# Performance work log

Hardware: AMD Instinct MI355X
Metric: run time of the kernel (lower is better)

The kernel has to match this reference:

```python
import jax, jax.numpy as jnp
import numpy as np
from jax import lax

K = 33  # avgpool kernel
P = 16  # padding
EPS = 1e-08


def _box_sum(x):
    # Sum over 33x33 windows, stride 1, zero padding 16 on H and W (NCHW).
    return lax.reduce_window(
        x, 0.0, lax.add,
        window_dimensions=(1, 1, K, K),
        window_strides=(1, 1, 1, 1),
        padding=((0, 0), (0, 0), (P, P), (P, P)),
    )


def setup_inputs() -> dict:
    key = jax.random.key(0)
    input_tensor = jax.random.normal(key, (64, 1, 80, 3000), dtype=jnp.float32)
    return {"input_tensor": input_tensor}


def reference(input_tensor):
    B, C, H, W = input_tensor.shape
    # count_include_pad=False: divide by number of VALID elements per window.
    counts = _box_sum(jnp.ones((1, 1, H, W), dtype=input_tensor.dtype))
    local_mean = _box_sum(input_tensor) / counts
    centered = input_tensor - local_mean
    local_var = _box_sum(centered * centered) / counts
    local_std = jnp.sqrt(local_var)
    return centered / (local_std + EPS)
```

## Files before the change

### kernel.cpp

```cpp
#include <hip/hip_runtime.h>
#include <hip/hip_bf16.h>
#include <math.h>

#define BB 64
#define HH 80
#define WW 3000
#define RAD 16
#define TW 80
#define NLOAD 112
#define XSW 112
#define HXS 116
#define NSTRIP 38
#define NT 1024
#define EPSF 1e-8f

#define XS_WORDS (HH * XSW)
#define HXP_OFF  XS_WORDS
#define HXP_WORDS (TW * HXS)
#define ICH_OFF  (XS_WORDS + HXP_WORDS)
#define TOT_WORDS (ICH_OFF + HH)

typedef float f32x2 __attribute__((ext_vector_type(2)));
typedef float f32x4 __attribute__((ext_vector_type(4)));

__device__ __forceinline__ float bflo(uint32_t w) { return __uint_as_float(w << 16); }
__device__ __forceinline__ float bfhi(uint32_t w) { return __uint_as_float(w & 0xffff0000u); }
__device__ __forceinline__ uint32_t packbf2(float lo, float hi) {
    union { __hip_bfloat162 h2; uint32_t u; } u;
    u.h2 = __hip_bfloat162(__float2bfloat16(lo), __float2bfloat16(hi));
    return u.u;
}
__device__ __forceinline__ f32x2 uw(uint32_t w) {
    f32x2 r; r.x = bflo(w); r.y = bfhi(w); return r;
}

#if defined(__has_builtin)
#if __has_builtin(__builtin_amdgcn_global_load_lds)
#define HAVE_GLL 1
__device__ __forceinline__ void gload_lds16(const float* g, float* l) {
    __builtin_amdgcn_global_load_lds(
        (const __attribute__((address_space(1))) void*)g,
        (__attribute__((address_space(3))) void*)l, 16, 0, 0);
}
#endif
#endif

#define E4(V, J) ((J) == 0 ? (V).x : ((J) == 1 ? (V).y : ((J) == 2 ? (V).z : (V).w)))
#define F48(Q) E4((Q) < 4 ? G0 : (Q) < 8 ? G1 : (Q) < 12 ? G2 : (Q) < 16 ? G3 : (Q) < 20 ? G4 : \
                  (Q) < 24 ? G5 : (Q) < 28 ? G6 : (Q) < 32 ? G7 : (Q) < 36 ? G8 : \
                  (Q) < 40 ? G9 : (Q) < 44 ? G10 : G11, (Q) & 3)
#define W48(Q) E4((Q) < 4 ? R0 : (Q) < 8 ? R1 : (Q) < 12 ? R2 : (Q) < 16 ? R3 : (Q) < 20 ? R4 : \
                  (Q) < 24 ? R5 : (Q) < 28 ? R6 : (Q) < 32 ? R7 : (Q) < 36 ? R8 : \
                  (Q) < 40 ? R9 : (Q) < 44 ? R10 : R11, (Q) & 3)
#define F16(K) E4((K) < 4 ? f0 : (K) < 8 ? f1 : (K) < 12 ? f2 : f3, (K) & 3)

__global__ __launch_bounds__(NT, 8)
void localnorm_kernel(const float* __restrict__ in, float* __restrict__ out) {
    extern __shared__ uint32_t smem[];
    float*    smemf = (float*)smem;
    uint32_t* Hxp   = smem + HXP_OFF;
    float*   inv_ch = (float*)(smem + ICH_OFF);

    const int t     = threadIdx.x;
    const int strip = blockIdx.x % NSTRIP;
    const int b     = blockIdx.x / NSTRIP;
    const int c0    = strip * TW;
    const float* inb = in + (size_t)b * (HH * WW);

    if (t < HH) {
        int lo = max(t - RAD, 0), hi = min(t + RAD, HH - 1);
        inv_ch[t] = 1.0f / (float)(hi - lo + 1);
    }
    if (t < 640) {
        const int col = t >> 3;
        const int c8  = t & 7;
        const int off = col * HXS + ((c8 < 4) ? (c8 * 4) : (96 + (c8 - 4) * 4));
        *(uint4*)(Hxp + off) = make_uint4(0u, 0u, 0u, 0u);
    }

    bool dma = false;
#ifdef HAVE_GLL
    dma = (c0 >= 16) && (c0 + NLOAD - 16 <= WW);
#endif
    if (dma) {
#ifdef HAVE_GLL
        const float* gsrc = inb + (c0 - 16);
        #pragma unroll
        for (int i = 0; i < 3; ++i) {
            const int ck = t + i * NT;
            if (i < 2 || ck < 2240) {
                const int row = ck / 28;
                const int m   = ck - row * 28;
                gload_lds16(gsrc + (size_t)row * WW + 4 * m, smemf + 4 * ck);
            }
        }
#endif
    } else {
        #pragma unroll
        for (int it = 0; it < 3; ++it) {
            const int id = t + it * NT;
            if (it < 2 || id < 2240) {
                const int row = id / 28;
                const int q   = id - row * 28;
                const int gc  = c0 - 16 + 4 * q;
                const float* rp = inb + (size_t)row * WW;
                f32x4 v;
                if (gc >= 0 && gc + 4 <= WW) {
                    v = *(const f32x4*)(rp + gc);
                } else {
                    v.x = (gc     >= 0 && gc     < WW) ? rp[gc]     : 0.f;
                    v.y = (gc + 1 >= 0 && gc + 1 < WW) ? rp[gc + 1] : 0.f;
                    v.z = (gc + 2 >= 0 && gc + 2 < WW) ? rp[gc + 2] : 0.f;
                    v.w = (gc + 3 >= 0 && gc + 3 < WW) ? rp[gc + 3] : 0.f;
                }
                *(f32x4*)(smemf + row * XSW + 4 * q) = v;
            }
        }
    }
    __syncthreads();

    {
        const int row = t % HH;
        const int seg = t / HH;
        if (seg < 5) {
            const float* xr = smemf + row * XSW + seg * 16;
            f32x4 G0  = *(const f32x4*)(xr);
            f32x4 G1  = *(const f32x4*)(xr + 4);
            f32x4 G2  = *(const f32x4*)(xr + 8);
            f32x4 G3  = *(const f32x4*)(xr + 12);
            f32x4 G4  = *(const f32x4*)(xr + 16);
            f32x4 G5  = *(const f32x4*)(xr + 20);
            f32x4 G6  = *(const f32x4*)(xr + 24);
            f32x4 G7  = *(const f32x4*)(xr + 28);
            f32x4 G8  = *(const f32x4*)(xr + 32);
            f32x4 G9  = *(const f32x4*)(xr + 36);
            f32x4 G10 = *(const f32x4*)(xr + 40);
            f32x4 G11 = *(const f32x4*)(xr + 44);
            float e32 = F48(32);
            float axA = e32, axB = 0.f;
            float qxA = e32 * e32, qxB = 0.f;
            #pragma unroll
            for (int q = 0; q < 32; q += 2) {
                float fa = F48(q), fb = F48(q + 1);
                axA += fa;                 axB += fb;
                qxA = fmaf(fa, fa, qxA);   qxB = fmaf(fb, fb, qxB);
            }
            float ax = axA + axB, axx = qxA + qxB;
            uint32_t* hw = Hxp + (seg * 16) * HXS + row + 16;
            #pragma unroll
            for (int k = 0; k < 8; ++k) {
                float fs = F48(2 * k), fe = F48(2 * k + 33);
                float a1x  = ax - fs + fe;
                float a1xx = fmaf(fe, fe, fmaf(-fs, fs, axx));
                hw[(2 * k) * HXS]     = packbf2(ax, axx);
                hw[(2 * k + 1) * HXS] = packbf2(a1x, a1xx);
                if (k != 7) {
                    float fs2 = F48(2 * k + 1), fe2 = F48(2 * k + 34);
                    ax  = a1x - fs2 + fe2;
                    axx = fmaf(fe2, fe2, fmaf(-fs2, fs2, a1xx));
                }
            }
        }
    }
    __syncthreads();

    {
        const int c    = t % TW;
        const int band = t / TW;
        const int gc   = c0 + c;
        if (band < 5 && gc < WW) {
            const int r0 = band * 16;
            const uint32_t* hp = Hxp + c * HXS + r0;
            uint4 R0  = *(const uint4*)(hp);
            uint4 R1  = *(const uint4*)(hp + 4);
            uint4 R2  = *(const uint4*)(hp + 8);
            uint4 R3  = *(const uint4*)(hp + 12);
            uint4 R4  = *(const uint4*)(hp + 16);
            uint4 R5  = *(const uint4*)(hp + 20);
            uint4 R6  = *(const uint4*)(hp + 24);
            uint4 R7  = *(const uint4*)(hp + 28);
            uint4 R8  = *(const uint4*)(hp + 32);
            uint4 R9  = *(const uint4*)(hp + 36);
            uint4 R10 = *(const uint4*)(hp + 40);
            uint4 R11 = *(const uint4*)(hp + 44);
            f32x2 aA = uw(W48(32));
            f32x2 aB; aB.x = 0.f; aB.y = 0.f;
            #pragma unroll
            for (int q = 0; q < 32; q += 2) {
                aA += uw(W48(q));
                aB += uw(W48(q + 1));
            }
            f32x2 acc = aA + aB;
            const float icw = 1.0f / (float)(min(gc + RAD, WW - 1) - max(gc - RAD, 0) + 1);
            f32x4 f0 = *(const f32x4*)(inv_ch + r0);
            f32x4 f1 = *(const f32x4*)(inv_ch + r0 + 4);
            f32x4 f2 = *(const f32x4*)(inv_ch + r0 + 8);
            f32x4 f3 = *(const f32x4*)(inv_ch + r0 + 12);
            float* outb = out + (size_t)b * (HH * WW);
            #pragma unroll
            for (int k = 0; k < 16; ++k) {
                const int r = r0 + k;
                const float ninv = F16(k) * icw;
                f32x2 me = acc * ninv;
                float var = fmaxf(me.y - me.x * me.x, 1e-24f);
#if defined(__has_builtin) && __has_builtin(__builtin_amdgcn_rsqf)
                float isd = __builtin_amdgcn_rsqf(var);
#else
                float isd = __builtin_amdgcn_rcpf(__builtin_amdgcn_sqrtf(var) + EPSF);
#endif
                float xv = smemf[r * XSW + c + 16];
                outb[(size_t)r * WW + gc] = (xv - me.x) * isd;
                if (k != 15) {
                    acc += uw(W48(k + 33)) - uw(W48(k));
                }
            }
        }
    }
}

extern "C" void kernel_launch(void* const* d_in, const int* in_sizes, int n_in,
                              void* d_out, int out_size, void* d_ws, size_t ws_size,
                              hipStream_t stream) {
    const float* in = (const float*)d_in[0];
    float* out = (float*)d_out;

    const size_t lds_bytes = (size_t)TOT_WORDS * sizeof(uint32_t);
    static bool attr_set = false;
    if (!attr_set) {
        (void)hipFuncSetAttribute((const void*)localnorm_kernel,
                                  hipFuncAttributeMaxDynamicSharedMemorySize,
                                  (int)lds_bytes);
        attr_set = true;
    }

    dim3 grid(BB * NSTRIP);
    dim3 block(NT);
    localnorm_kernel<<<grid, block, lds_bytes, stream>>>(in, out);
}
```

Baseline: 35.76 us.

## Use persistent blocks with double-buffered async prefetch of narrower strips

Converts the one-block-per-strip launch into a persistent grid of 512 blocks that loop over work items. Each block prefetches the next strip's input into a second LDS buffer with global_load_lds while it computes the current strip. Strip width drops from 80 to 48 columns, so the 32-column halo is a larger fraction of each load. Only 3 of 16 waves run the horizontal pass and 10 run the vertical pass, so thread utilisation per phase falls and redundant halo reads grow, in exchange for overlapping load latency with compute.

Measured after the change: 45.52 us. +27.3%, slower.

```diff
diff --git a/kernel.cpp b/kernel.cpp
--- a/kernel.cpp
+++ b/kernel.cpp
@@ -6,18 +6,20 @@
 #define HH 80
 #define WW 3000
 #define RAD 16
-#define TW 80
-#define NLOAD 112
-#define XSW 112
+#define TW 48
+#define NLOAD 80
+#define XSW 80
 #define HXS 116
-#define NSTRIP 38
+#define NSTRIP 63
+#define NITEMS (BB * NSTRIP)
+#define NBLK 512
 #define NT 1024
 #define EPSF 1e-8f
 
-#define XS_WORDS (HH * XSW)
-#define HXP_OFF  XS_WORDS
-#define HXP_WORDS (TW * HXS)
-#define ICH_OFF  (XS_WORDS + HXP_WORDS)
+#define XSA_OFF 0
+#define XSB_OFF (HH * XSW)
+#define HXP_OFF (2 * HH * XSW)
+#define ICH_OFF (HXP_OFF + TW * HXS)
 #define TOT_WORDS (ICH_OFF + HH)
 
 typedef float f32x2 __attribute__((ext_vector_type(2)));
@@ -45,14 +47,54 @@
 #endif
 #endif
 
+__device__ __forceinline__ void stage_item(const float* __restrict__ in, int w, float* xbuf, int t) {
+    const int b     = w / NSTRIP;
+    const int strip = w - b * NSTRIP;
+    const int c0    = strip * TW;
+    const float* inb = in + (size_t)b * (HH * WW);
+#ifdef HAVE_GLL
+    if ((c0 >= 16) && (c0 - 16 + NLOAD <= WW)) {
+        const float* gsrc = inb + (c0 - 16);
+        {
+            const int ck = t;
+            const int row = ck / 20, m = ck - row * 20;
+            gload_lds16(gsrc + (size_t)row * WW + 4 * m, xbuf + 4 * ck);
+        }
+        if (t < 576) {
+            const int ck = t + NT;
+            const int row = ck / 20, m = ck - row * 20;
+            gload_lds16(gsrc + (size_t)row * WW + 4 * m, xbuf + 4 * ck);
+        }
+        return;
+    }
+#endif
+    #pragma unroll
+    for (int it = 0; it < 2; ++it) {
+        const int id = t + it * NT;
+        if (it == 0 || id < 1600) {
+            const int row = id / 20, q = id - row * 20;
+            const int gc  = c0 - 16 + 4 * q;
+            const float* rp = inb + (size_t)row * WW;
+            f32x4 v;
+            if (gc >= 0 && gc + 4 <= WW) {
+                v = *(const f32x4*)(rp + gc);
+            } else {
+                v.x = (gc     >= 0 && gc     < WW) ? rp[gc]     : 0.f;
+                v.y = (gc + 1 >= 0 && gc + 1 < WW) ? rp[gc + 1] : 0.f;
+                v.z = (gc + 2 >= 0 && gc + 2 < WW) ? rp[gc + 2] : 0.f;
+                v.w = (gc + 3 >= 0 && gc + 3 < WW) ? rp[gc + 3] : 0.f;
+            }
+            *(f32x4*)(xbuf + 4 * id) = v;
+        }
+    }
+}
+
 #define E4(V, J) ((J) == 0 ? (V).x : ((J) == 1 ? (V).y : ((J) == 2 ? (V).z : (V).w)))
 #define F48(Q) E4((Q) < 4 ? G0 : (Q) < 8 ? G1 : (Q) < 12 ? G2 : (Q) < 16 ? G3 : (Q) < 20 ? G4 : \
                   (Q) < 24 ? G5 : (Q) < 28 ? G6 : (Q) < 32 ? G7 : (Q) < 36 ? G8 : \
                   (Q) < 40 ? G9 : (Q) < 44 ? G10 : G11, (Q) & 3)
-#define W48(Q) E4((Q) < 4 ? R0 : (Q) < 8 ? R1 : (Q) < 12 ? R2 : (Q) < 16 ? R3 : (Q) < 20 ? R4 : \
-                  (Q) < 24 ? R5 : (Q) < 28 ? R6 : (Q) < 32 ? R7 : (Q) < 36 ? R8 : \
-                  (Q) < 40 ? R9 : (Q) < 44 ? R10 : R11, (Q) & 3)
-#define F16(K) E4((K) < 4 ? f0 : (K) < 8 ? f1 : (K) < 12 ? f2 : f3, (K) & 3)
+#define W40(Q) E4((Q) < 4 ? v0 : (Q) < 8 ? v1 : (Q) < 12 ? v2 : (Q) < 16 ? v3 : (Q) < 20 ? v4 : \
+                  (Q) < 24 ? v5 : (Q) < 28 ? v6 : (Q) < 32 ? v7 : (Q) < 36 ? v8 : v9, (Q) & 3)
 
 __global__ __launch_bounds__(NT, 8)
 void localnorm_kernel(const float* __restrict__ in, float* __restrict__ out) {
@@ -60,161 +102,132 @@
     float*    smemf = (float*)smem;
     uint32_t* Hxp   = smem + HXP_OFF;
     float*   inv_ch = (float*)(smem + ICH_OFF);
-
-    const int t     = threadIdx.x;
-    const int strip = blockIdx.x % NSTRIP;
-    const int b     = blockIdx.x / NSTRIP;
-    const int c0    = strip * TW;
-    const float* inb = in + (size_t)b * (HH * WW);
+    float*   XsA    = smemf + XSA_OFF;
+    float*   XsB    = smemf + XSB_OFF;
+
+    const int t   = threadIdx.x;
+    const int bid = blockIdx.x;
 
     if (t < HH) {
         int lo = max(t - RAD, 0), hi = min(t + RAD, HH - 1);
         inv_ch[t] = 1.0f / (float)(hi - lo + 1);
     }
-    if (t < 640) {
+    if (t < 384) {
         const int col = t >> 3;
         const int c8  = t & 7;
         const int off = col * HXS + ((c8 < 4) ? (c8 * 4) : (96 + (c8 - 4) * 4));
         *(uint4*)(Hxp + off) = make_uint4(0u, 0u, 0u, 0u);
     }
 
-    bool dma = false;
-#ifdef HAVE_GLL
-    dma = (c0 >= 16) && (c0 + NLOAD - 16 <= WW);
-#endif
-    if (dma) {
-#ifdef HAVE_GLL
-        const float* gsrc = inb + (c0 - 16);
-        #pragma unroll
-        for (int i = 0; i < 3; ++i) {
-            const int ck = t + i * NT;
-            if (i < 2 || ck < 2240) {
-                const int row = ck / 28;
-                const int m   = ck - row * 28;
-                gload_lds16(gsrc + (size_t)row * WW + 4 * m, smemf + 4 * ck);
+    stage_item(in, bid, XsA, t);
+    __syncthreads();
+
+    int cur = 0;
+    #pragma unroll 1
+    for (int w = bid; w < NITEMS; w += NBLK) {
+        float* Xs = cur ? XsB : XsA;
+        float* Xn = cur ? XsA : XsB;
+        if (w + NBLK < NITEMS) stage_item(in, w + NBLK, Xn, t);
+
+        const int b     = w / NSTRIP;
+        const int strip = w - b * NSTRIP;
+        const int c0    = strip * TW;
+
+        {
+            const int row = t % HH;
+            const int seg = t / HH;
+            if (seg < 3) {
+                const float* xr = Xs + row * XSW + seg * 16;
+                f32x4 G0  = *(const f32x4*)(xr);
+                f32x4 G1  = *(const f32x4*)(xr + 4);
+                f32x4 G2  = *(const f32x4*)(xr + 8);
+                f32x4 G3  = *(const f32x4*)(xr + 12);
+                f32x4 G4  = *(const f32x4*)(xr + 16);
+                f32x4 G5  = *(const f32x4*)(xr + 20);
+                f32x4 G6  = *(const f32x4*)(xr + 24);
+                f32x4 G7  = *(const f32x4*)(xr + 28);
+                f32x4 G8  = *(const f32x4*)(xr + 32);
+                f32x4 G9  = *(const f32x4*)(xr + 36);
+                f32x4 G10 = *(const f32x4*)(xr + 40);
+                f32x4 G11 = *(const f32x4*)(xr + 44);
+                float e32 = F48(32);
+                float axA = e32, axB = 0.f;
+                float qxA = e32 * e32, qxB = 0.f;
+                #pragma unroll
+                for (int q = 0; q < 32; q += 2) {
+                    float fa = F48(q), fb = F48(q + 1);
+                    axA += fa;                 axB += fb;
+                    qxA = fmaf(fa, fa, qxA);   qxB = fmaf(fb, fb, qxB);
+                }
+                float ax = axA + axB, axx = qxA + qxB;
+                uint32_t* hw = Hxp + (seg * 16) * HXS + row + 16;
+                #pragma unroll
+                for (int k = 0; k < 8; ++k) {
+                    float fs = F48(2 * k), fe = F48(2 * k + 33);
+                    float a1x  = ax - fs + fe;
+                    float a1xx = fmaf(fe, fe, fmaf(-fs, fs, axx));
+                    hw[(2 * k) * HXS]     = packbf2(ax, axx);
+                    hw[(2 * k + 1) * HXS] = packbf2(a1x, a1xx);
+                    if (k != 7) {
+                        float fs2 = F48(2 * k + 1), fe2 = F48(2 * k + 34);
+                        ax  = a1x - fs2 + fe2;
+                        axx = fmaf(fe2, fe2, fmaf(-fs2, fs2, a1xx));
+                    }
+                }
             }
         }
-#endif
-    } else {
-        #pragma unroll
-        for (int it = 0; it < 3; ++it) {
-            const int id = t + it * NT;
-            if (it < 2 || id < 2240) {
-                const int row = id / 28;
-                const int q   = id - row * 28;
-                const int gc  = c0 - 16 + 4 * q;
-                const float* rp = inb + (size_t)row * WW;
-                f32x4 v;
-                if (gc >= 0 && gc + 4 <= WW) {
-                    v = *(const f32x4*)(rp + gc);
-                } else {
-                    v.x = (gc     >= 0 && gc     < WW) ? rp[gc]     : 0.f;
-                    v.y = (gc + 1 >= 0 && gc + 1 < WW) ? rp[gc + 1] : 0.f;
-                    v.z = (gc + 2 >= 0 && gc + 2 < WW) ? rp[gc + 2] : 0.f;
-                    v.w = (gc + 3 >= 0 && gc + 3 < WW) ? rp[gc + 3] : 0.f;
-                }
-                *(f32x4*)(smemf + row * XSW + 4 * q) = v;
+        __syncthreads();
+
+        {
+            const int c    = t % TW;
+            const int band = t / TW;
+            const int gc   = c0 + c;
+            if (band < 10 && gc < WW) {
+                const int r0 = band * 8;
+                const uint32_t* hp = Hxp + c * HXS + r0;
+                uint4 v0 = *(const uint4*)(hp);
+                uint4 v1 = *(const uint4*)(hp + 4);
+                uint4 v2 = *(const uint4*)(hp + 8);
+                uint4 v3 = *(const uint4*)(hp + 12);
+                uint4 v4 = *(const uint4*)(hp + 16);
+                uint4 v5 = *(const uint4*)(hp + 20);
+                uint4 v6 = *(const uint4*)(hp + 24);
+                uint4 v7 = *(const uint4*)(hp + 28);
+                uint4 v8 = *(const uint4*)(hp + 32);
+                uint4 v9 = *(const uint4*)(hp + 36);
+                f32x2 aA = uw(W40(32));
+                f32x2 aB; aB.x = 0.f; aB.y = 0.f;
+                #pragma unroll
+                for (int q = 0; q < 32; q += 2) {
+                    aA += uw(W40(q));
+                    aB += uw(W40(q + 1));
+                }
+                f32x2 acc = aA + aB;
+                const float icw = 1.0f / (float)(min(gc + RAD, WW - 1) - max(gc - RAD, 0) + 1);
+                f32x4 f4a = *(const f32x4*)(inv_ch + r0);
+                f32x4 f4b = *(const f32x4*)(inv_ch + r0 + 4);
+                float* outb = out + (size_t)b * (HH * WW);
+                #pragma unroll
+                for (int k = 0; k < 8; ++k) {
+                    const int r = r0 + k;
+                    const float ninv = E4(k < 4 ? f4a : f4b, k & 3) * icw;
+                    f32x2 me = acc * ninv;
+                    float var = fmaxf(me.y - me.x * me.x, 1e-24f);
+#if defined(__has_builtin) && __has_builtin(__builtin_amdgcn_rsqf)
+                    float isd = __builtin_amdgcn_rsqf(var);
+#else
+                    float isd = __builtin_amdgcn_rcpf(__builtin_amdgcn_sqrtf(var) + EPSF);
+#endif
+                    float xv = Xs[r * XSW + c + 16];
+                    outb[(size_t)r * WW + gc] = (xv - me.x) * isd;
+                    if (k != 7) {
+                        acc += uw(W40(k + 33)) - uw(W40(k));
+                    }
+                }
             }
         }
-    }
-    __syncthreads();
-
-    {
-        const int row = t % HH;
-        const int seg = t / HH;
-        if (seg < 5) {
-            const float* xr = smemf + row * XSW + seg * 16;
-            f32x4 G0  = *(const f32x4*)(xr);
-            f32x4 G1  = *(const f32x4*)(xr + 4);
-            f32x4 G2  = *(const f32x4*)(xr + 8);
-            f32x4 G3  = *(const f32x4*)(xr + 12);
-            f32x4 G4  = *(const f32x4*)(xr + 16);
-            f32x4 G5  = *(const f32x4*)(xr + 20);
-            f32x4 G6  = *(const f32x4*)(xr + 24);
-            f32x4 G7  = *(const f32x4*)(xr + 28);
-            f32x4 G8  = *(const f32x4*)(xr + 32);
-            f32x4 G9  = *(const f32x4*)(xr + 36);
-            f32x4 G10 = *(const f32x4*)(xr + 40);
-            f32x4 G11 = *(const f32x4*)(xr + 44);
-            float e32 = F48(32);
-            float axA = e32, axB = 0.f;
-            float qxA = e32 * e32, qxB = 0.f;
-            #pragma unroll
-            for (int q = 0; q < 32; q += 2) {
-                float fa = F48(q), fb = F48(q + 1);
-                axA += fa;                 axB += fb;
-                qxA = fmaf(fa, fa, qxA);   qxB = fmaf(fb, fb, qxB);
-            }
-            float ax = axA + axB, axx = qxA + qxB;
-            uint32_t* hw = Hxp + (seg * 16) * HXS + row + 16;
-            #pragma unroll
-            for (int k = 0; k < 8; ++k) {
-                float fs = F48(2 * k), fe = F48(2 * k + 33);
-                float a1x  = ax - fs + fe;
-                float a1xx = fmaf(fe, fe, fmaf(-fs, fs, axx));
-                hw[(2 * k) * HXS]     = packbf2(ax, axx);
-                hw[(2 * k + 1) * HXS] = packbf2(a1x, a1xx);
-                if (k != 7) {
-                    float fs2 = F48(2 * k + 1), fe2 = F48(2 * k + 34);
-                    ax  = a1x - fs2 + fe2;
-                    axx = fmaf(fe2, fe2, fmaf(-fs2, fs2, a1xx));
-                }
-            }
-        }
-    }
-    __syncthreads();
-
-    {
-        const int c    = t % TW;
-        const int band = t / TW;
-        const int gc   = c0 + c;
-        if (band < 5 && gc < WW) {
-            const int r0 = band * 16;
-            const uint32_t* hp = Hxp + c * HXS + r0;
-            uint4 R0  = *(const uint4*)(hp);
-            uint4 R1  = *(const uint4*)(hp + 4);
-            uint4 R2  = *(const uint4*)(hp + 8);
-            uint4 R3  = *(const uint4*)(hp + 12);
-            uint4 R4  = *(const uint4*)(hp + 16);
-            uint4 R5  = *(const uint4*)(hp + 20);
-            uint4 R6  = *(const uint4*)(hp + 24);
-            uint4 R7  = *(const uint4*)(hp + 28);
-            uint4 R8  = *(const uint4*)(hp + 32);
-            uint4 R9  = *(const uint4*)(hp + 36);
-            uint4 R10 = *(const uint4*)(hp + 40);
-            uint4 R11 = *(const uint4*)(hp + 44);
-            f32x2 aA = uw(W48(32));
-            f32x2 aB; aB.x = 0.f; aB.y = 0.f;
-            #pragma unroll
-            for (int q = 0; q < 32; q += 2) {
-                aA += uw(W48(q));
-                aB += uw(W48(q + 1));
-            }
-            f32x2 acc = aA + aB;
-            const float icw = 1.0f / (float)(min(gc + RAD, WW - 1) - max(gc - RAD, 0) + 1);
-            f32x4 f0 = *(const f32x4*)(inv_ch + r0);
-            f32x4 f1 = *(const f32x4*)(inv_ch + r0 + 4);
-            f32x4 f2 = *(const f32x4*)(inv_ch + r0 + 8);
-            f32x4 f3 = *(const f32x4*)(inv_ch + r0 + 12);
-            float* outb = out + (size_t)b * (HH * WW);
-            #pragma unroll
-            for (int k = 0; k < 16; ++k) {
-                const int r = r0 + k;
-                const float ninv = F16(k) * icw;
-                f32x2 me = acc * ninv;
-                float var = fmaxf(me.y - me.x * me.x, 1e-24f);
-#if defined(__has_builtin) && __has_builtin(__builtin_amdgcn_rsqf)
-                float isd = __builtin_amdgcn_rsqf(var);
-#else
-                float isd = __builtin_amdgcn_rcpf(__builtin_amdgcn_sqrtf(var) + EPSF);
-#endif
-                float xv = smemf[r * XSW + c + 16];
-                outb[(size_t)r * WW + gc] = (xv - me.x) * isd;
-                if (k != 15) {
-                    acc += uw(W48(k + 33)) - uw(W48(k));
-                }
-            }
-        }
+        __syncthreads();
+        cur ^= 1;
     }
 }
 
@@ -233,7 +246,7 @@
         attr_set = true;
     }
 
-    dim3 grid(BB * NSTRIP);
+    dim3 grid(NBLK);
     dim3 block(NT);
     localnorm_kernel<<<grid, block, lds_bytes, stream>>>(in, out);
 }
```

## Split input tile load into two halves and overlap with horizontal pass

Applied to the files above, without the earlier changes.

The 80-row input tile is now loaded in two halves of 40 rows each. The horizontal running-sum pass for the first half runs while the second half's global-to-LDS loads are in flight, and the second half is processed after an extra barrier. The aim is to hide part of the global load latency behind compute inside each block. In exchange it adds a barrier and changes the thread-to-(row, segment) mapping, which alters LDS access patterns. Each half also uses only 200 active threads.

After: 37.70 us. 5.4% more time.

```diff
diff --git a/kernel.cpp b/kernel.cpp
--- a/kernel.cpp
+++ b/kernel.cpp
@@ -45,6 +45,45 @@
 #endif
 #endif
 
+#ifdef HAVE_GLL
+__device__ __forceinline__ void dma_half(const float* __restrict__ gsrc, float* __restrict__ lds,
+                                         int t, int base) {
+    {
+        const int ck  = base + t;
+        const int row = ck / 28, m = ck - row * 28;
+        gload_lds16(gsrc + (size_t)row * WW + 4 * m, lds + 4 * ck);
+    }
+    if (t < 96) {
+        const int ck  = base + 1024 + t;
+        const int row = ck / 28, m = ck - row * 28;
+        gload_lds16(gsrc + (size_t)row * WW + 4 * m, lds + 4 * ck);
+    }
+}
+#endif
+
+__device__ __forceinline__ void fb_half(const float* __restrict__ inb, int c0,
+                                        float* __restrict__ lds, int t, int base) {
+    #pragma unroll
+    for (int it = 0; it < 2; ++it) {
+        if (it == 0 || t < 96) {
+            const int id  = base + t + it * NT;
+            const int row = id / 28, q = id - row * 28;
+            const int gc  = c0 - 16 + 4 * q;
+            const float* rp = inb + (size_t)row * WW;
+            f32x4 v;
+            if (gc >= 0 && gc + 4 <= WW) {
+                v = *(const f32x4*)(rp + gc);
+            } else {
+                v.x = (gc     >= 0 && gc     < WW) ? rp[gc]     : 0.f;
+                v.y = (gc + 1 >= 0 && gc + 1 < WW) ? rp[gc + 1] : 0.f;
+                v.z = (gc + 2 >= 0 && gc + 2 < WW) ? rp[gc + 2] : 0.f;
+                v.w = (gc + 3 >= 0 && gc + 3 < WW) ? rp[gc + 3] : 0.f;
+            }
+            *(f32x4*)(lds + 4 * id) = v;
+        }
+    }
+}
+
 #define E4(V, J) ((J) == 0 ? (V).x : ((J) == 1 ? (V).y : ((J) == 2 ? (V).z : (V).w)))
 #define F48(Q) E4((Q) < 4 ? G0 : (Q) < 8 ? G1 : (Q) < 12 ? G2 : (Q) < 16 ? G3 : (Q) < 20 ? G4 : \
                   (Q) < 24 ? G5 : (Q) < 28 ? G6 : (Q) < 32 ? G7 : (Q) < 36 ? G8 : \
@@ -54,6 +93,47 @@
                   (Q) < 40 ? R9 : (Q) < 44 ? R10 : R11, (Q) & 3)
 #define F16(K) E4((K) < 4 ? f0 : (K) < 8 ? f1 : (K) < 12 ? f2 : f3, (K) & 3)
 
+__device__ __forceinline__ void p2_body(const float* __restrict__ smemf,
+                                        uint32_t* __restrict__ Hxp, int row, int seg) {
+    const float* xr = smemf + row * XSW + seg * 16;
+    f32x4 G0  = *(const f32x4*)(xr);
+    f32x4 G1  = *(const f32x4*)(xr + 4);
+    f32x4 G2  = *(const f32x4*)(xr + 8);
+    f32x4 G3  = *(const f32x4*)(xr + 12);
+    f32x4 G4  = *(const f32x4*)(xr + 16);
+    f32x4 G5  = *(const f32x4*)(xr + 20);
+    f32x4 G6  = *(const f32x4*)(xr + 24);
+    f32x4 G7  = *(const f32x4*)(xr + 28);
+    f32x4 G8  = *(const f32x4*)(xr + 32);
+    f32x4 G9  = *(const f32x4*)(xr + 36);
+    f32x4 G10 = *(const f32x4*)(xr + 40);
+    f32x4 G11 = *(const f32x4*)(xr + 44);
+    float e32 = F48(32);
+    float axA = e32, axB = 0.f;
+    float qxA = e32 * e32, qxB = 0.f;
+    #pragma unroll
+    for (int q = 0; q < 32; q += 2) {
+        float fa = F48(q), fb = F48(q + 1);
+        axA += fa;                 axB += fb;
+        qxA = fmaf(fa, fa, qxA);   qxB = fmaf(fb, fb, qxB);
+    }
+    float ax = axA + axB, axx = qxA + qxB;
+    uint32_t* hw = Hxp + (seg * 16) * HXS + row + 16;
+    #pragma unroll
+    for (int k = 0; k < 8; ++k) {
+        float fs = F48(2 * k), fe = F48(2 * k + 33);
+        float a1x  = ax - fs + fe;
+        float a1xx = fmaf(fe, fe, fmaf(-fs, fs, axx));
+        hw[(2 * k) * HXS]     = packbf2(ax, axx);
+        hw[(2 * k + 1) * HXS] = packbf2(a1x, a1xx);
+        if (k != 7) {
+            float fs2 = F48(2 * k + 1), fe2 = F48(2 * k + 34);
+            ax  = a1x - fs2 + fe2;
+            axx = fmaf(fe2, fe2, fmaf(-fs2, fs2, a1xx));
+        }
+    }
+}
+
 __global__ __launch_bounds__(NT, 8)
 void localnorm_kernel(const float* __restrict__ in, float* __restrict__ out) {
     extern __shared__ uint32_t smem[];
@@ -80,88 +160,31 @@
 
     bool dma = false;
 #ifdef HAVE_GLL
-    dma = (c0 >= 16) && (c0 + NLOAD - 16 <= WW);
-#endif
+    dma = (c0 >= 16) && (c0 - 16 + NLOAD <= WW);
+#endif
+
     if (dma) {
 #ifdef HAVE_GLL
-        const float* gsrc = inb + (c0 - 16);
-        #pragma unroll
-        for (int i = 0; i < 3; ++i) {
-            const int ck = t + i * NT;
-            if (i < 2 || ck < 2240) {
-                const int row = ck / 28;
-                const int m   = ck - row * 28;
-                gload_lds16(gsrc + (size_t)row * WW + 4 * m, smemf + 4 * ck);
-            }
-        }
+        dma_half(inb + (c0 - 16), smemf, t, 0);
 #endif
     } else {
-        #pragma unroll
-        for (int it = 0; it < 3; ++it) {
-            const int id = t + it * NT;
-            if (it < 2 || id < 2240) {
-                const int row = id / 28;
-                const int q   = id - row * 28;
-                const int gc  = c0 - 16 + 4 * q;
-                const float* rp = inb + (size_t)row * WW;
-                f32x4 v;
-                if (gc >= 0 && gc + 4 <= WW) {
-                    v = *(const f32x4*)(rp + gc);
-                } else {
-                    v.x = (gc     >= 0 && gc     < WW) ? rp[gc]     : 0.f;
-                    v.y = (gc + 1 >= 0 && gc + 1 < WW) ? rp[gc + 1] : 0.f;
-                    v.z = (gc + 2 >= 0 && gc + 2 < WW) ? rp[gc + 2] : 0.f;
-                    v.w = (gc + 3 >= 0 && gc + 3 < WW) ? rp[gc + 3] : 0.f;
-                }
-                *(f32x4*)(smemf + row * XSW + 4 * q) = v;
-            }
-        }
+        fb_half(inb, c0, smemf, t, 0);
     }
     __syncthreads();
 
+    if (dma) {
+#ifdef HAVE_GLL
+        dma_half(inb + (c0 - 16), smemf, t, 1120);
+#endif
+    } else {
+        fb_half(inb, c0, smemf, t, 1120);
+    }
     {
-        const int row = t % HH;
-        const int seg = t / HH;
-        if (seg < 5) {
-            const float* xr = smemf + row * XSW + seg * 16;
-            f32x4 G0  = *(const f32x4*)(xr);
-            f32x4 G1  = *(const f32x4*)(xr + 4);
-            f32x4 G2  = *(const f32x4*)(xr + 8);
-            f32x4 G3  = *(const f32x4*)(xr + 12);
-            f32x4 G4  = *(const f32x4*)(xr + 16);
-            f32x4 G5  = *(const f32x4*)(xr + 20);
-            f32x4 G6  = *(const f32x4*)(xr + 24);
-            f32x4 G7  = *(const f32x4*)(xr + 28);
-            f32x4 G8  = *(const f32x4*)(xr + 32);
-            f32x4 G9  = *(const f32x4*)(xr + 36);
-            f32x4 G10 = *(const f32x4*)(xr + 40);
-            f32x4 G11 = *(const f32x4*)(xr + 44);
-            float e32 = F48(32);
-            float axA = e32, axB = 0.f;
-            float qxA = e32 * e32, qxB = 0.f;
-            #pragma unroll
-            for (int q = 0; q < 32; q += 2) {
-                float fa = F48(q), fb = F48(q + 1);
-                axA += fa;                 axB += fb;
-                qxA = fmaf(fa, fa, qxA);   qxB = fmaf(fb, fb, qxB);
-            }
-            float ax = axA + axB, axx = qxA + qxB;
-            uint32_t* hw = Hxp + (seg * 16) * HXS + row + 16;
-            #pragma unroll
-            for (int k = 0; k < 8; ++k) {
-                float fs = F48(2 * k), fe = F48(2 * k + 33);
-                float a1x  = ax - fs + fe;
-                float a1xx = fmaf(fe, fe, fmaf(-fs, fs, axx));
-                hw[(2 * k) * HXS]     = packbf2(ax, axx);
-                hw[(2 * k + 1) * HXS] = packbf2(a1x, a1xx);
-                if (k != 7) {
-                    float fs2 = F48(2 * k + 1), fe2 = F48(2 * k + 34);
-                    ax  = a1x - fs2 + fe2;
-                    axx = fmaf(fe2, fe2, fmaf(-fs2, fs2, a1xx));
-                }
-            }
-        }
-    }
+        if (t < 200) p2_body(smemf, Hxp, t / 5, t % 5);
+    }
+    __syncthreads();
+
+    if (t >= 200 && t < 400) p2_body(smemf, Hxp, t / 5, t % 5);
     __syncthreads();
 
     {
```
